# Kernel optimization log

Hardware: AMD Instinct MI355X
Metric: run time of the kernel (lower is better)

The kernel has to match this reference:

```python
import jax, jax.numpy as jnp
import numpy as np
from jax import lax

GRID = 200      # _FIXED_GRID_LEN
SOFT_K = 50.0   # _SOFT_MASK_K
BN_EPS = 1e-5


def setup_inputs() -> dict:
    key = jax.random.key(0)
    ks = jax.random.split(key, 12)
    B, L = 8192, 2001
    f32 = jnp.float32
    inp = {
        'phase': jax.random.uniform(ks[0], (B, L), f32, -1.0, 1.0),
        'primary_flux': 0.01 * jax.random.normal(ks[1], (B, L), f32),
        'secondary_flux': 0.01 * jax.random.normal(ks[2], (B, L), f32),
        'odd_even_diff': 0.01 * jax.random.normal(ks[3], (B, L), f32),
        # TaylorGateLayerV8 params
        'A': jnp.asarray(0.01, f32),
        'Bp': jnp.asarray(1.0, f32),
        't0': jnp.asarray(0.0, f32),
        # BatchNorm1d(4), eval mode (running stats)
        'bn_gamma': jnp.ones((4,), f32),
        'bn_beta': jnp.zeros((4,), f32),
        'bn_mean': jnp.zeros((4,), f32),
        'bn_var': jnp.ones((4,), f32),
        # Conv1d(4,8,7) / Conv1d(8,16,5)
        'conv1_w': 0.1 * jax.random.normal(ks[4], (8, 4, 7), f32),
        'conv1_b': jnp.zeros((8,), f32),
        'conv2_w': 0.1 * jax.random.normal(ks[5], (16, 8, 5), f32),
        'conv2_b': jnp.zeros((16,), f32),
        # Linear(21, 1)
        'fc_w': 0.1 * jax.random.normal(ks[6], (1, 21), f32),
        'fc_b': jnp.zeros((1,), f32),
    }
    return inp


def _conv1d(x, w, b, pad):
    # x: (B, C, L), w: (O, C, K)
    y = lax.conv_general_dilated(x, w, window_strides=(1,), padding=[(pad, pad)],
                                 dimension_numbers=('NCH', 'OIH', 'NCH'))
    return y + b[None, :, None]


def _interp_linear_ac(x, out_len):
    # torch F.interpolate(mode='linear', align_corners=True) on (B, L) -> (B, out_len)
    L = x.shape[1]
    pos = jnp.linspace(0.0, L - 1.0, out_len)
    i0 = jnp.floor(pos).astype(jnp.int32)
    i1 = jnp.minimum(i0 + 1, L - 1)
    w = (pos - i0).astype(x.dtype)
    return x[:, i0] * (1.0 - w) + x[:, i1] * w


def reference(phase, primary_flux, secondary_flux, odd_even_diff,
              A, Bp, t0, bn_gamma, bn_beta, bn_mean, bn_var,
              conv1_w, conv1_b, conv2_w, conv2_b, fc_w, fc_b):
    # --- TaylorGateLayerV8: 2nd-order Taylor U-shape transit template ---
    gate = -A * jnp.clip(1.0 - Bp * (phase - t0) ** 2, 0.0, None)

    # --- CNN branch ---
    x = jnp.stack([gate, primary_flux, secondary_flux, odd_even_diff], axis=1)  # (B,4,L)
    inv = bn_gamma / jnp.sqrt(bn_var + BN_EPS)
    x = x * inv[None, :, None] + (bn_beta - bn_mean * inv)[None, :, None]
    x = jax.nn.relu(_conv1d(x, conv1_w, conv1_b, 3))
    x = jax.nn.relu(_conv1d(x, conv2_w, conv2_b, 2))
    cnn_out = jnp.mean(x, axis=2)  # AdaptiveAvgPool1d(1) -> (B,16)

    # --- shape features ---
    batch = primary_flux.shape[0]
    A_abs = jnp.abs(A) + 1e-8
    depth = jnp.clip(-primary_flux, 0.0, None)
    depth_norm = depth / A_abs
    depth_rs = _interp_linear_ac(depth, GRID)  # (B, 200)
    dx = 2.0 / (GRID - 1)                       # trapz over linspace(-1,1,200)
    auc_raw = dx * (jnp.sum(depth_rs, axis=1) - 0.5 * (depth_rs[:, 0] + depth_rs[:, -1]))
    auc_norm = auc_raw / A_abs
    dip_all = jax.nn.sigmoid(SOFT_K * (depth_norm - 0.1))
    flat_bot = jax.nn.sigmoid(SOFT_K * (depth_norm - 0.8))
    ingress = dip_all - flat_bot
    total = 1.0 - dip_all + ingress + flat_bot + 1e-8
    ingress = ingress / total
    flat_bot = flat_bot / total
    t14 = jnp.mean(ingress + flat_bot, axis=1) + 1e-8
    t12_t14 = jnp.mean(ingress, axis=1) / t14
    flat_bottom = jnp.mean(flat_bot, axis=1)
    B_bcast = jnp.broadcast_to(Bp, (batch,)).astype(depth.dtype)
    shape = jnp.stack([B_bcast, auc_raw, auc_norm, t12_t14, flat_bottom], axis=1)  # (B,5)

    features = jnp.concatenate([cnn_out, shape], axis=1)  # (B,21)
    logits = features @ fc_w.T + fc_b
    return jax.nn.sigmoid(logits)
```

## Files before the change

### kernel.cpp

```cpp
#include <hip/hip_runtime.h>
#include <math.h>

#define L_LEN 2001
#define CCH 672
#define XR  704
#define NTB 43
#define NTC 42

typedef __attribute__((ext_vector_type(8))) short bf16x8;
typedef __attribute__((ext_vector_type(4))) float f32x4;
#if __has_builtin(__builtin_amdgcn_cvt_pk_bf16_f32)
typedef __attribute__((ext_vector_type(2))) __bf16 bf16x2_t;
#endif

union FragU { unsigned u[4]; uint2 u2[2]; uint4 u4; bf16x8 v; };

__device__ __forceinline__ unsigned short f2bf(float f) {
    unsigned u = __builtin_bit_cast(unsigned, f);
    u += 0x7fffu + ((u >> 16) & 1u);
    return (unsigned short)(u >> 16);
}
__device__ __forceinline__ unsigned bfpack(float lo, float hi) {
#if __has_builtin(__builtin_amdgcn_cvt_pk_bf16_f32)
    bf16x2_t r = __builtin_amdgcn_cvt_pk_bf16_f32(lo, hi);
    return __builtin_bit_cast(unsigned, r);
#else
    unsigned ul = __builtin_bit_cast(unsigned, lo);
    unsigned uh = __builtin_bit_cast(unsigned, hi);
    ul += 0x7fffu + ((ul >> 16) & 1u);
    uh += 0x7fffu + ((uh >> 16) & 1u);
    return __builtin_amdgcn_perm(uh, ul, 0x07060302);
#endif
}
__device__ __forceinline__ float fast_rcp(float x) { return __builtin_amdgcn_rcpf(x); }
__device__ __forceinline__ float fexp2(float x) {
#if __has_builtin(__builtin_amdgcn_exp2f)
    return __builtin_amdgcn_exp2f(x);
#else
    return __expf(x * 0.69314718f);
#endif
}

__global__ __launch_bounds__(256, 6)
void taylor_cnn_v8_mfma(const float* __restrict__ phase, const float* __restrict__ primary,
                        const float* __restrict__ secondary, const float* __restrict__ oddeven,
                        const float* __restrict__ pA, const float* __restrict__ pBp,
                        const float* __restrict__ pT0,
                        const float* __restrict__ bng, const float* __restrict__ bnb,
                        const float* __restrict__ bnm, const float* __restrict__ bnv,
                        const float* __restrict__ w1, const float* __restrict__ b1,
                        const float* __restrict__ w2, const float* __restrict__ b2,
                        const float* __restrict__ fcw, const float* __restrict__ fcb,
                        float* __restrict__ out, int nrows)
{
    __shared__ __align__(16) unsigned int xs_i[XR * 2];
    __shared__ __align__(16) unsigned int y1_i[XR * 4];
    __shared__ float redA[4][16];
    __shared__ float redB[4][3];

    const int tid = threadIdx.x;
    const int row = blockIdx.x;
    const long base = (long)row * L_LEN;
    (void)nrows;

    const int lane = tid & 63;
    const int wid  = tid >> 6;
    const int n    = lane & 15;
    const int quad = lane >> 4;

    const float A  = pA[0];
    const float Bp = pBp[0];
    const float t0 = pT0[0];
    const float A_abs = fabsf(A) + 1e-8f;
    const float rAabs = 1.0f / A_abs;
    const float nBp  = -Bp;
    const float cExp = -72.134766f * rAabs;

    float inv1, inv2, inv3, gInv0, off0, off1, off2, off3;
    {
        float iv0 = bng[0] / sqrtf(bnv[0] + 1e-5f);
        float iv1 = bng[1] / sqrtf(bnv[1] + 1e-5f);
        float iv2 = bng[2] / sqrtf(bnv[2] + 1e-5f);
        float iv3 = bng[3] / sqrtf(bnv[3] + 1e-5f);
        gInv0 = -A * iv0;
        inv1 = iv1; inv2 = iv2; inv3 = iv3;
        off0 = bnb[0] - bnm[0] * iv0;
        off1 = bnb[1] - bnm[1] * iv1;
        off2 = bnb[2] - bnm[2] * iv2;
        off3 = bnb[3] - bnm[3] * iv3;
    }

    bf16x8 a1;
#pragma unroll
    for (int jp = 0; jp < 8; ++jp) {
        int j = quad + 4 * (jp >> 2);
        int c = jp & 3;
        float v = (n < 8 && j < 7) ? w1[(n * 4 + c) * 7 + j] : 0.0f;
        a1[jp] = (short)f2bf(v);
    }
    bf16x8 a20, a21;
#pragma unroll
    for (int jp = 0; jp < 8; ++jp) {
        float v0 = w2[(n * 8 + jp) * 5 + quad];
        float v1 = (quad + 4 < 5) ? w2[(n * 8 + jp) * 5 + quad + 4] : 0.0f;
        a20[jp] = (short)f2bf(v0);
        a21[jp] = (short)f2bf(v1);
    }
    f32x4 cb1, cb2;
#pragma unroll
    for (int r = 0; r < 4; ++r) {
        cb1[r] = b1[(quad * 4 + r) & 7];
        cb2[r] = b2[quad * 4 + r];
    }

    float s_ing = 0.0f, s_fb = 0.0f;
    float m0 = 0.f, m1 = 0.f, m2 = 0.f, m3 = 0.f;

    float s_auc = 0.0f;
    if (tid < 200) {
        float pos = (float)tid * (2000.0f / 199.0f);
        int i0 = (int)pos;
        if (i0 > 2000) i0 = 2000;
        int i1 = (i0 + 1 < L_LEN) ? i0 + 1 : 2000;
        float w  = pos - (float)i0;
        float d0 = fmaxf(-primary[base + i0], 0.f);
        float d1 = fmaxf(-primary[base + i1], 0.f);
        float v  = d0 * (1.0f - w) + d1 * w;
        float wt = (tid == 0 || tid == 199) ? 0.5f : 1.0f;
        s_auc = v * wt;
    }

    auto aRec = [&](int m, int p, bool chk) {
        bool valid = true, core = true;
        int pc = p;
        if (chk) {
            valid = ((unsigned)p < (unsigned)L_LEN);
            core  = valid && (m >= 16) && (m < 16 + CCH);
            pc = min(max(p, 0), L_LEN - 1);
        }
        float ph = phase[base + pc];
        float pf = primary[base + pc];
        float sf = secondary[base + pc];
        float oe = oddeven[base + pc];
        float dd = ph - t0;
        float g  = fmaxf(fmaf(dd * dd, nBp, 1.0f), 0.0f);
        float x0 = fmaf(g,  gInv0, off0);
        float x1 = fmaf(pf, inv1, off1);
        float x2 = fmaf(sf, inv2, off2);
        float x3 = fmaf(oe, inv3, off3);
        unsigned d0 = bfpack(x0, x1);
        unsigned d1 = bfpack(x2, x3);
        if (chk && !valid) { d0 = 0u; d1 = 0u; }
        *(uint2*)&xs_i[2 * m] = make_uint2(d0, d1);
        float depth = fmaxf(-pf, 0.0f);
        float e   = fexp2(depth * cExp);
        float dip = fast_rcp(fmaf(e, 148.413159f, 1.0f));
        float fb  = fast_rcp(fmaf(e, 2.35385267e17f, 1.0f));
        float ing = dip - fb;
        if (chk && !core) { ing = 0.f; fb = 0.f; }
        s_ing += ing;
        s_fb  += fb;
    };

    auto stageA = [&](int c0) {
        const int pb = c0 - 16;
        aRec(tid,       pb + tid,       true);
        aRec(tid + 256, pb + tid + 256, false);
        if (tid < 192) aRec(tid + 512, pb + tid + 512, true);
    };

    auto stageB = [&](int c0, int tLo, int tFrom) {
        for (int t = wid; t < NTB; t += 4) {
            int qb = 16 * t + n + quad + 5;
            FragU bu;
            bu.u2[0] = *(const uint2*)&xs_i[2 * qb];
            bu.u2[1] = *(const uint2*)&xs_i[2 * (qb + 4)];
            f32x4 d = __builtin_amdgcn_mfma_f32_16x16x32_bf16(a1, bu.v, cb1, 0, 0, 0);
            if (lane < 32) {
                int q = 16 * t + n;
                unsigned w0, w1_;
                if (t == tLo || t >= tFrom) {
                    int p = c0 - 8 + q;
                    bool ok = ((unsigned)p < (unsigned)L_LEN);
                    w0  = ok ? bfpack(fmaxf(d[0], 0.f), fmaxf(d[1], 0.f)) : 0u;
                    w1_ = ok ? bfpack(fmaxf(d[2], 0.f), fmaxf(d[3], 0.f)) : 0u;
                } else {
                    w0  = bfpack(fmaxf(d[0], 0.f), fmaxf(d[1], 0.f));
                    w1_ = bfpack(fmaxf(d[2], 0.f), fmaxf(d[3], 0.f));
                }
                *(uint2*)&y1_i[4 * q + 2 * quad] = make_uint2(w0, w1_);
            }
        }
    };

    auto stageC = [&](int maskT) {
        for (int t = wid; t < NTC; t += 4) {
            int q = 16 * t + n + quad + 6;
            FragU u0, u1;
            u0.u4 = *(const uint4*)&y1_i[4 * q];
            u1.u4 = *(const uint4*)&y1_i[4 * (q + 4)];
            f32x4 d = __builtin_amdgcn_mfma_f32_16x16x32_bf16(a20, u0.v, cb2, 0, 0, 0);
            d = __builtin_amdgcn_mfma_f32_16x16x32_bf16(a21, u1.v, d, 0, 0, 0);
            if (t == maskT) {
                float msk = (n == 0) ? 1.0f : 0.0f;
                m0 = fmaf(fmaxf(d[0], 0.f), msk, m0);
                m1 = fmaf(fmaxf(d[1], 0.f), msk, m1);
                m2 = fmaf(fmaxf(d[2], 0.f), msk, m2);
                m3 = fmaf(fmaxf(d[3], 0.f), msk, m3);
            } else {
                m0 += fmaxf(d[0], 0.f);
                m1 += fmaxf(d[1], 0.f);
                m2 += fmaxf(d[2], 0.f);
                m3 += fmaxf(d[3], 0.f);
            }
        }
    };

    stageA(0);
    __syncthreads();
    stageB(0, 0, 99);
    __syncthreads();
    stageA(CCH);
    stageC(-1);
    __syncthreads();
    stageB(CCH, -1, 99);
    __syncthreads();
    stageA(2 * CCH);
    stageC(-1);
    __syncthreads();
    stageB(2 * CCH, -1, 41);
    __syncthreads();
    stageC(41);

#pragma unroll
    for (int dlt = 8; dlt >= 1; dlt >>= 1) {
        m0 += __shfl_xor(m0, dlt);
        m1 += __shfl_xor(m1, dlt);
        m2 += __shfl_xor(m2, dlt);
        m3 += __shfl_xor(m3, dlt);
    }
    if ((lane & 15) == 0) {
        redA[wid][quad * 4 + 0] = m0;
        redA[wid][quad * 4 + 1] = m1;
        redA[wid][quad * 4 + 2] = m2;
        redA[wid][quad * 4 + 3] = m3;
    }
#pragma unroll
    for (int dlt = 32; dlt >= 1; dlt >>= 1) {
        s_ing += __shfl_xor(s_ing, dlt);
        s_fb  += __shfl_xor(s_fb,  dlt);
        s_auc += __shfl_xor(s_auc, dlt);
    }
    if (lane == 0) {
        redB[wid][0] = s_ing;
        redB[wid][1] = s_fb;
        redB[wid][2] = s_auc;
    }
    __syncthreads();

    if (tid == 0) {
        float logit = fcb[0];
#pragma unroll
        for (int oc = 0; oc < 16; ++oc) {
            float s = redA[0][oc] + redA[1][oc] + redA[2][oc] + redA[3][oc];
            logit += (s / 2001.0f) * fcw[oc];
        }
        float Sing = redB[0][0] + redB[1][0] + redB[2][0] + redB[3][0];
        float Sfb  = redB[0][1] + redB[1][1] + redB[2][1] + redB[3][1];
        float Sauc = redB[0][2] + redB[1][2] + redB[2][2] + redB[3][2];

        float auc_raw  = (float)(2.0 / 199.0) * Sauc;
        float auc_norm = auc_raw / A_abs;
        float m_ing = Sing / 2001.0f;
        float m_fb  = Sfb  / 2001.0f;
        float t14   = (Sing + Sfb) / 2001.0f + 1e-8f;
        float t12   = m_ing / t14;

        logit += Bp       * fcw[16]
               + auc_raw  * fcw[17]
               + auc_norm * fcw[18]
               + t12      * fcw[19]
               + m_fb     * fcw[20];

        out[row] = 1.0f / (1.0f + expf(-logit));
    }
}

extern "C" void kernel_launch(void* const* d_in, const int* in_sizes, int n_in,
                              void* d_out, int out_size, void* d_ws, size_t ws_size,
                              hipStream_t stream) {
    const float* phase     = (const float*)d_in[0];
    const float* primary   = (const float*)d_in[1];
    const float* secondary = (const float*)d_in[2];
    const float* oddeven   = (const float*)d_in[3];
    const float* pA        = (const float*)d_in[4];
    const float* pBp       = (const float*)d_in[5];
    const float* pT0       = (const float*)d_in[6];
    const float* bng       = (const float*)d_in[7];
    const float* bnb       = (const float*)d_in[8];
    const float* bnm       = (const float*)d_in[9];
    const float* bnv       = (const float*)d_in[10];
    const float* w1        = (const float*)d_in[11];
    const float* b1        = (const float*)d_in[12];
    const float* w2        = (const float*)d_in[13];
    const float* b2        = (const float*)d_in[14];
    const float* fcw       = (const float*)d_in[15];
    const float* fcb       = (const float*)d_in[16];
    float* out = (float*)d_out;

    int nrows = in_sizes[0] / L_LEN;
    dim3 grid(nrows), block(256);
    hipLaunchKernelGGL(taylor_cnn_v8_mfma, grid, block, 0, stream,
                       phase, primary, secondary, oddeven, pA, pBp, pT0,
                       bng, bnb, bnm, bnv, w1, b1, w2, b2, fcw, fcb, out, nrows);
}
```

Baseline: 309.1 us.

## Assign one row per wavefront, removing block barriers and shared reductions

Each 64-lane wavefront now processes a whole row by itself, in nine chunks of 224 positions with private LDS buffers, where before a 256-thread block shared one row. This removes every __syncthreads and the cross-wave shared-memory reduction, and the final FC dot product is folded into wave shuffles. In exchange each wave runs all conv tiles serially, and the occupancy hint drops from 6 to 4 blocks per CU, so load-latency hiding now depends on more independent rows per CU and may suffer.

```diff
diff --git a/kernel.cpp b/kernel.cpp
--- a/kernel.cpp
+++ b/kernel.cpp
@@ -2,10 +2,12 @@
 #include <math.h>
 
 #define L_LEN 2001
-#define CCH 672
-#define XR  704
-#define NTB 43
-#define NTC 42
+#define CCH 224
+#define NCH 9
+#define XRECS 256
+#define YRECS 240
+#define NTB 15
+#define NTC 14
 
 typedef __attribute__((ext_vector_type(8))) short bf16x8;
 typedef __attribute__((ext_vector_type(4))) float f32x4;
@@ -41,8 +43,8 @@
 #endif
 }
 
-__global__ __launch_bounds__(256, 6)
-void taylor_cnn_v8_mfma(const float* __restrict__ phase, const float* __restrict__ primary,
+__global__ __launch_bounds__(256, 4)
+void taylor_cnn_v9_wave(const float* __restrict__ phase, const float* __restrict__ primary,
                         const float* __restrict__ secondary, const float* __restrict__ oddeven,
                         const float* __restrict__ pA, const float* __restrict__ pBp,
                         const float* __restrict__ pT0,
@@ -53,20 +55,21 @@
                         const float* __restrict__ fcw, const float* __restrict__ fcb,
                         float* __restrict__ out, int nrows)
 {
-    __shared__ __align__(16) unsigned int xs_i[XR * 2];
-    __shared__ __align__(16) unsigned int y1_i[XR * 4];
-    __shared__ float redA[4][16];
-    __shared__ float redB[4][3];
+    __shared__ __align__(16) unsigned int xs_i[4][XRECS * 2];
+    __shared__ __align__(16) unsigned int y1_i[4][YRECS * 4];
 
     const int tid = threadIdx.x;
-    const int row = blockIdx.x;
+    const int l   = tid & 63;
+    const int wid = tid >> 6;
+    const int row = blockIdx.x * 4 + wid;
+    if (row >= nrows) return;
     const long base = (long)row * L_LEN;
-    (void)nrows;
-
-    const int lane = tid & 63;
-    const int wid  = tid >> 6;
-    const int n    = lane & 15;
-    const int quad = lane >> 4;
+
+    unsigned int* xs = xs_i[wid];
+    unsigned int* y1 = y1_i[wid];
+
+    const int n    = l & 15;
+    const int quad = l >> 4;
 
     const float A  = pA[0];
     const float Bp = pBp[0];
@@ -112,36 +115,37 @@
         cb1[r] = b1[(quad * 4 + r) & 7];
         cb2[r] = b2[quad * 4 + r];
     }
+    float fw0 = fcw[quad * 4 + 0];
+    float fw1 = fcw[quad * 4 + 1];
+    float fw2 = fcw[quad * 4 + 2];
+    float fw3 = fcw[quad * 4 + 3];
 
     float s_ing = 0.0f, s_fb = 0.0f;
     float m0 = 0.f, m1 = 0.f, m2 = 0.f, m3 = 0.f;
 
     float s_auc = 0.0f;
-    if (tid < 200) {
-        float pos = (float)tid * (2000.0f / 199.0f);
-        int i0 = (int)pos;
-        if (i0 > 2000) i0 = 2000;
-        int i1 = (i0 + 1 < L_LEN) ? i0 + 1 : 2000;
-        float w  = pos - (float)i0;
-        float d0 = fmaxf(-primary[base + i0], 0.f);
-        float d1 = fmaxf(-primary[base + i1], 0.f);
-        float v  = d0 * (1.0f - w) + d1 * w;
-        float wt = (tid == 0 || tid == 199) ? 0.5f : 1.0f;
-        s_auc = v * wt;
-    }
-
-    auto aRec = [&](int m, int p, bool chk) {
-        bool valid = true, core = true;
-        int pc = p;
-        if (chk) {
-            valid = ((unsigned)p < (unsigned)L_LEN);
-            core  = valid && (m >= 16) && (m < 16 + CCH);
-            pc = min(max(p, 0), L_LEN - 1);
+#pragma unroll
+    for (int k = 0; k < 4; ++k) {
+        int s = l + 64 * k;
+        if (k < 3 || l < 8) {
+            float pos = (float)s * (2000.0f / 199.0f);
+            int i0 = (int)pos;
+            if (i0 > 2000) i0 = 2000;
+            int i1 = (i0 + 1 < L_LEN) ? i0 + 1 : 2000;
+            float w  = pos - (float)i0;
+            float d0 = fmaxf(-primary[base + i0], 0.f);
+            float d1 = fmaxf(-primary[base + i1], 0.f);
+            float v  = d0 * (1.0f - w) + d1 * w;
+            float wt = (s == 0 || s == 199) ? 0.5f : 1.0f;
+            s_auc += v * wt;
         }
-        float ph = phase[base + pc];
-        float pf = primary[base + pc];
-        float sf = secondary[base + pc];
-        float oe = oddeven[base + pc];
+    }
+
+    auto aRec = [&](int m, int p, bool valid, bool core) {
+        float ph = phase[base + p];
+        float pf = primary[base + p];
+        float sf = secondary[base + p];
+        float oe = oddeven[base + p];
         float dd = ph - t0;
         float g  = fmaxf(fmaf(dd * dd, nBp, 1.0f), 0.0f);
         float x0 = fmaf(g,  gInv0, off0);
@@ -150,36 +154,50 @@
         float x3 = fmaf(oe, inv3, off3);
         unsigned d0 = bfpack(x0, x1);
         unsigned d1 = bfpack(x2, x3);
-        if (chk && !valid) { d0 = 0u; d1 = 0u; }
-        *(uint2*)&xs_i[2 * m] = make_uint2(d0, d1);
+        if (!valid) { d0 = 0u; d1 = 0u; }
+        *(uint2*)&xs[2 * m] = make_uint2(d0, d1);
         float depth = fmaxf(-pf, 0.0f);
         float e   = fexp2(depth * cExp);
         float dip = fast_rcp(fmaf(e, 148.413159f, 1.0f));
         float fb  = fast_rcp(fmaf(e, 2.35385267e17f, 1.0f));
         float ing = dip - fb;
-        if (chk && !core) { ing = 0.f; fb = 0.f; }
+        if (!core) { ing = 0.f; fb = 0.f; }
         s_ing += ing;
         s_fb  += fb;
     };
 
-    auto stageA = [&](int c0) {
+#pragma unroll 1
+    for (int ch = 0; ch < NCH; ++ch) {
+        const int c0 = ch * CCH;
         const int pb = c0 - 16;
-        aRec(tid,       pb + tid,       true);
-        aRec(tid + 256, pb + tid + 256, false);
-        if (tid < 192) aRec(tid + 512, pb + tid + 512, true);
-    };
-
-    auto stageB = [&](int c0, int tLo, int tFrom) {
-        for (int t = wid; t < NTB; t += 4) {
+
+        {
+            bool v0  = (ch > 0) || (l >= 16);
+            bool co0 = (l >= 16);
+            int  p0  = pb + l;            if (p0 < 0) p0 = 0;
+            int  p3  = pb + l + 192;
+            bool v3  = (ch < NCH - 1) || (l < 33);
+            bool co3 = v3 && (l < 48);
+            if (p3 > 2000) p3 = 2000;
+            aRec(l,        p0,           v0,   co0);
+            aRec(l + 64,   pb + l + 64,  true, true);
+            aRec(l + 128,  pb + l + 128, true, true);
+            aRec(l + 192,  p3,           v3,   co3);
+        }
+
+        const bool bLo   = (ch == 0);
+        const int  bFrom = (ch == NCH - 1) ? 13 : 99;
+#pragma unroll 2
+        for (int t = 0; t < NTB; ++t) {
             int qb = 16 * t + n + quad + 5;
             FragU bu;
-            bu.u2[0] = *(const uint2*)&xs_i[2 * qb];
-            bu.u2[1] = *(const uint2*)&xs_i[2 * (qb + 4)];
+            bu.u2[0] = *(const uint2*)&xs[2 * qb];
+            bu.u2[1] = *(const uint2*)&xs[2 * (qb + 4)];
             f32x4 d = __builtin_amdgcn_mfma_f32_16x16x32_bf16(a1, bu.v, cb1, 0, 0, 0);
-            if (lane < 32) {
+            if (l < 32) {
                 int q = 16 * t + n;
                 unsigned w0, w1_;
-                if (t == tLo || t >= tFrom) {
+                if ((bLo && t == 0) || t >= bFrom) {
                     int p = c0 - 8 + q;
                     bool ok = ((unsigned)p < (unsigned)L_LEN);
                     w0  = ok ? bfpack(fmaxf(d[0], 0.f), fmaxf(d[1], 0.f)) : 0u;
@@ -188,17 +206,17 @@
                     w0  = bfpack(fmaxf(d[0], 0.f), fmaxf(d[1], 0.f));
                     w1_ = bfpack(fmaxf(d[2], 0.f), fmaxf(d[3], 0.f));
                 }
-                *(uint2*)&y1_i[4 * q + 2 * quad] = make_uint2(w0, w1_);
+                *(uint2*)&y1[4 * q + 2 * quad] = make_uint2(w0, w1_);
             }
         }
-    };
-
-    auto stageC = [&](int maskT) {
-        for (int t = wid; t < NTC; t += 4) {
+
+        const int maskT = (ch == NCH - 1) ? 13 : -1;
+#pragma unroll 2
+        for (int t = 0; t < NTC; ++t) {
             int q = 16 * t + n + quad + 6;
             FragU u0, u1;
-            u0.u4 = *(const uint4*)&y1_i[4 * q];
-            u1.u4 = *(const uint4*)&y1_i[4 * (q + 4)];
+            u0.u4 = *(const uint4*)&y1[4 * q];
+            u1.u4 = *(const uint4*)&y1[4 * (q + 4)];
             f32x4 d = __builtin_amdgcn_mfma_f32_16x16x32_bf16(a20, u0.v, cb2, 0, 0, 0);
             d = __builtin_amdgcn_mfma_f32_16x16x32_bf16(a21, u1.v, d, 0, 0, 0);
             if (t == maskT) {
@@ -214,23 +232,7 @@
                 m3 += fmaxf(d[3], 0.f);
             }
         }
-    };
-
-    stageA(0);
-    __syncthreads();
-    stageB(0, 0, 99);
-    __syncthreads();
-    stageA(CCH);
-    stageC(-1);
-    __syncthreads();
-    stageB(CCH, -1, 99);
-    __syncthreads();
-    stageA(2 * CCH);
-    stageC(-1);
-    __syncthreads();
-    stageB(2 * CCH, -1, 41);
-    __syncthreads();
-    stageC(41);
+    }
 
 #pragma unroll
     for (int dlt = 8; dlt >= 1; dlt >>= 1) {
@@ -239,41 +241,24 @@
         m2 += __shfl_xor(m2, dlt);
         m3 += __shfl_xor(m3, dlt);
     }
-    if ((lane & 15) == 0) {
-        redA[wid][quad * 4 + 0] = m0;
-        redA[wid][quad * 4 + 1] = m1;
-        redA[wid][quad * 4 + 2] = m2;
-        redA[wid][quad * 4 + 3] = m3;
-    }
+    float part = m0 * fw0 + m1 * fw1 + m2 * fw2 + m3 * fw3;
+    part = (n == 0) ? part : 0.0f;
+    part += __shfl_xor(part, 16);
+    part += __shfl_xor(part, 32);
 #pragma unroll
     for (int dlt = 32; dlt >= 1; dlt >>= 1) {
         s_ing += __shfl_xor(s_ing, dlt);
         s_fb  += __shfl_xor(s_fb,  dlt);
         s_auc += __shfl_xor(s_auc, dlt);
     }
-    if (lane == 0) {
-        redB[wid][0] = s_ing;
-        redB[wid][1] = s_fb;
-        redB[wid][2] = s_auc;
-    }
-    __syncthreads();
-
-    if (tid == 0) {
-        float logit = fcb[0];
-#pragma unroll
-        for (int oc = 0; oc < 16; ++oc) {
-            float s = redA[0][oc] + redA[1][oc] + redA[2][oc] + redA[3][oc];
-            logit += (s / 2001.0f) * fcw[oc];
-        }
-        float Sing = redB[0][0] + redB[1][0] + redB[2][0] + redB[3][0];
-        float Sfb  = redB[0][1] + redB[1][1] + redB[2][1] + redB[3][1];
-        float Sauc = redB[0][2] + redB[1][2] + redB[2][2] + redB[3][2];
-
-        float auc_raw  = (float)(2.0 / 199.0) * Sauc;
+
+    if (l == 0) {
+        float logit = fcb[0] + part * (1.0f / 2001.0f);
+        float auc_raw  = (float)(2.0 / 199.0) * s_auc;
         float auc_norm = auc_raw / A_abs;
-        float m_ing = Sing / 2001.0f;
-        float m_fb  = Sfb  / 2001.0f;
-        float t14   = (Sing + Sfb) / 2001.0f + 1e-8f;
+        float m_ing = s_ing / 2001.0f;
+        float m_fb  = s_fb  / 2001.0f;
+        float t14   = (s_ing + s_fb) / 2001.0f + 1e-8f;
         float t12   = m_ing / t14;
 
         logit += Bp       * fcw[16]
@@ -309,8 +294,8 @@
     float* out = (float*)d_out;
 
     int nrows = in_sizes[0] / L_LEN;
-    dim3 grid(nrows), block(256);
-    hipLaunchKernelGGL(taylor_cnn_v8_mfma, grid, block, 0, stream,
+    dim3 grid((nrows + 3) / 4), block(256);
+    hipLaunchKernelGGL(taylor_cnn_v9_wave, grid, block, 0, stream,
                        phase, primary, secondary, oddeven, pA, pBp, pT0,
                        bng, bnb, bnm, bnv, w1, b1, w2, b2, fcw, fcb, out, nrows);
 }
```

New measurement: 300.1 us. 1.03x faster.
